# Optimization experiments

Measured on AMD Instinct MI355X. Metric: run time of the kernel, lower is better.

The kernel has to match this reference:

```python
import jax, jax.numpy as jnp
import numpy as np

ALPHA = 32.0
RANK = 256
SCALE = ALPHA / RANK


def setup_inputs() -> dict:
    key = jax.random.key(0)
    k1, k2, k3, k4 = jax.random.split(key, 4)
    x = jax.random.normal(k1, (4, 2048, 4096), dtype=jnp.float32)
    A = jax.random.normal(k2, (256, 4096), dtype=jnp.float32)   # (rank, in)
    B = jax.random.normal(k3, (4096, 256), dtype=jnp.float32)   # (out, rank)
    d_A = jnp.ones((256,), dtype=jnp.float32)                    # init = ones (as in module)
    d_B = jax.random.normal(k4, (4096,), dtype=jnp.float32)      # perturbed for a nontrivial test
    return {"x": x, "A": A, "B": B, "d_A": d_A, "d_B": d_B}


def reference(x, A, B, d_A, d_B):
    # Effective weight: diag(d_B) @ B @ diag(d_A) @ A  -> (out, in)
    scaled_A = d_A[:, None] * A                 # (rank, in)
    BA = B @ scaled_A                            # (out, in)
    W_vera = d_B[:, None] * BA                   # (out, in)
    # out = x @ W_vera.T * scale  -> (..., out)
    return jnp.einsum('bsi,oi->bso', x, W_vera) * SCALE
```

## Files before the change

kernel.cpp:

```cpp
#include <hip/hip_runtime.h>
#include <hip/hip_bf16.h>


#define SCALE_F 0.125f
#define M_TOT 8192
#define K_IN 4096
#define RANK 256
#define N_OUT 4096
#define S_SPLIT 4
#define KC 1024

typedef __bf16 bf16_t;
typedef __bf16 bf16x8 __attribute__((ext_vector_type(8)));
typedef __bf16 bf16x4 __attribute__((ext_vector_type(4)));
typedef float f32x4 __attribute__((ext_vector_type(4)));

typedef __attribute__((address_space(3))) unsigned int lds_u32_t;
typedef const __attribute__((address_space(1))) unsigned int glob_u32_t;

__device__ __forceinline__ void async16(const void* g, void* l) {
    __builtin_amdgcn_global_load_lds((glob_u32_t*)g, (lds_u32_t*)l, 16, 0, 0);
}

__global__ __launch_bounds__(256) void conv_A(const float* __restrict__ A,
                                              const float* __restrict__ dA,
                                              bf16_t* __restrict__ Ab) {
    int idx = blockIdx.x * 256 + threadIdx.x;
    float4 v = ((const float4*)A)[idx];
    float s = dA[idx >> 10];
    bf16x4 o;
    o.x = (bf16_t)(v.x * s); o.y = (bf16_t)(v.y * s);
    o.z = (bf16_t)(v.z * s); o.w = (bf16_t)(v.w * s);
    ((bf16x4*)Ab)[idx] = o;
}

__global__ __launch_bounds__(256) void conv_B(const float* __restrict__ B,
                                              bf16_t* __restrict__ Bb) {
    int idx = blockIdx.x * 256 + threadIdx.x;
    float4 v = ((const float4*)B)[idx];
    bf16x4 o;
    o.x = (bf16_t)v.x; o.y = (bf16_t)v.y; o.z = (bf16_t)v.z; o.w = (bf16_t)v.w;
    ((bf16x4*)Bb)[idx] = o;
}

__global__ __launch_bounds__(256) void gemm1(const float* __restrict__ x,
                                             const bf16_t* __restrict__ Ab,
                                             bf16_t* __restrict__ part) {
    __shared__ bf16_t sX[2][64 * 64];
    __shared__ bf16_t sA[2][128 * 64];
    const int tid = threadIdx.x;
    const int lane = tid & 63, wave = tid >> 6;
    const int wm = wave >> 1, wn = wave & 1;
    const int l15 = lane & 15, quad = lane >> 4;
    const int bm = blockIdx.x * 64;
    const int bn = blockIdx.y * 128;
    const int k0 = blockIdx.z * KC;

    f32x4 acc[2][4];
    const f32x4 zero = {0.f, 0.f, 0.f, 0.f};
    #pragma unroll
    for (int i = 0; i < 2; i++)
        #pragma unroll
        for (int j = 0; j < 4; j++) acc[i][j] = zero;

    f32x4 xr[2][2];

    auto issue_x = [&](int kk) {
        #pragma unroll
        for (int c = 0; c < 2; c++) {
            int idx = c * 256 + tid;
            int row = idx >> 3, sl = idx & 7;
            const float* sp = &x[(size_t)(bm + row) * K_IN + kk + sl * 8];
            xr[c][0] = *(const f32x4*)sp;
            xr[c][1] = *(const f32x4*)(sp + 4);
        }
    };
    auto stage_a = [&](int b, int kk) {
        #pragma unroll
        for (int c = 0; c < 4; c++) {
            int idx = c * 256 + tid;
            int row = idx >> 3, sl = idx & 7;
            async16(&Ab[(size_t)(bn + row) * K_IN + kk + ((sl ^ (row & 7)) << 3)],
                    &sA[b][idx * 8]);
        }
    };
    auto write_x = [&](int b) {
        #pragma unroll
        for (int c = 0; c < 2; c++) {
            int idx = c * 256 + tid;
            int row = idx >> 3, sl = idx & 7;
            bf16x8 o;
            #pragma unroll
            for (int e = 0; e < 4; e++) {
                o[e]     = (bf16_t)xr[c][0][e];
                o[e + 4] = (bf16_t)xr[c][1][e];
            }
            *(bf16x8*)&sX[b][row * 64 + ((sl ^ (row & 7)) << 3)] = o;
        }
    };
    auto compute = [&](int b) {
        #pragma unroll
        for (int ks = 0; ks < 2; ks++) {
            bf16x8 af[2], bfr[4];
            #pragma unroll
            for (int i = 0; i < 2; i++) {
                int row = wm * 32 + i * 16 + l15;
                af[i] = *(const bf16x8*)&sX[b][row * 64 + ((((ks << 2) | quad) ^ (row & 7)) << 3)];
            }
            #pragma unroll
            for (int j = 0; j < 4; j++) {
                int row = wn * 64 + j * 16 + l15;
                bfr[j] = *(const bf16x8*)&sA[b][row * 64 + ((((ks << 2) | quad) ^ (row & 7)) << 3)];
            }
            #pragma unroll
            for (int i = 0; i < 2; i++)
                #pragma unroll
                for (int j = 0; j < 4; j++)
                    acc[i][j] = __builtin_amdgcn_mfma_f32_16x16x32_bf16(af[i], bfr[j], acc[i][j], 0, 0, 0);
        }
    };

    issue_x(k0);
    stage_a(0, k0);
    write_x(0);
    __syncthreads();

    int cur = 0;
    for (int it = 1; it < KC / 64; ++it) {
        const int nxt = cur ^ 1;
        const int kk = k0 + it * 64;
        issue_x(kk);
        stage_a(nxt, kk);
        compute(cur);
        write_x(nxt);
        __syncthreads();
        cur = nxt;
    }
    compute(cur);

    bf16_t* p = part + (size_t)blockIdx.z * (M_TOT * RANK);
    #pragma unroll
    for (int i = 0; i < 2; i++) {
        #pragma unroll
        for (int j = 0; j < 4; j++) {
            int col = bn + wn * 64 + j * 16 + l15;
            #pragma unroll
            for (int r = 0; r < 4; r++) {
                int row = bm + wm * 32 + i * 16 + quad * 4 + r;
                p[(size_t)row * RANK + col] = (bf16_t)acc[i][j][r];
            }
        }
    }
}

__global__ __launch_bounds__(256) void reduce_t(const bf16_t* __restrict__ part,
                                                bf16_t* __restrict__ t) {
    int i = (blockIdx.x * 256 + threadIdx.x) * 8;
    float s[8] = {0.f, 0.f, 0.f, 0.f, 0.f, 0.f, 0.f, 0.f};
    #pragma unroll
    for (int z = 0; z < S_SPLIT; z++) {
        bf16x8 v = *(const bf16x8*)&part[(size_t)z * M_TOT * RANK + i];
        #pragma unroll
        for (int e = 0; e < 8; e++) s[e] += (float)v[e];
    }
    bf16x8 o;
    #pragma unroll
    for (int e = 0; e < 8; e++) o[e] = (bf16_t)s[e];
    *(bf16x8*)&t[i] = o;
}

__global__ __launch_bounds__(256) void gemm2(const bf16_t* __restrict__ t,
                                             const bf16_t* __restrict__ Bb,
                                             const float* __restrict__ dB,
                                             float* __restrict__ out) {
    __shared__ bf16_t sT[2][128 * 64];
    __shared__ bf16_t sB[2][128 * 64];
    const int tid = threadIdx.x;
    const int lane = tid & 63, wave = tid >> 6;
    const int wm = wave >> 1, wn = wave & 1;
    const int l15 = lane & 15, quad = lane >> 4;
    const int bm = blockIdx.x * 128;
    const int bn = blockIdx.y * 128;

    f32x4 acc[4][4];
    const f32x4 zero = {0.f, 0.f, 0.f, 0.f};
    #pragma unroll
    for (int i = 0; i < 4; i++)
        #pragma unroll
        for (int j = 0; j < 4; j++) acc[i][j] = zero;

    auto stage = [&](int b, int kt) {
        #pragma unroll
        for (int c = 0; c < 4; c++) {
            int idx = c * 256 + tid;
            int row = idx >> 3, sl = idx & 7;
            async16(&t[(size_t)(bm + row) * RANK + kt + ((sl ^ (row & 7)) << 3)],
                    &sT[b][idx * 8]);
        }
        #pragma unroll
        for (int c = 0; c < 4; c++) {
            int idx = c * 256 + tid;
            int row = idx >> 3, sl = idx & 7;
            async16(&Bb[(size_t)(bn + row) * RANK + kt + ((sl ^ (row & 7)) << 3)],
                    &sB[b][idx * 8]);
        }
    };
    auto compute = [&](int b) {
        #pragma unroll
        for (int ks = 0; ks < 2; ks++) {
            bf16x8 af[4], bfr[4];
            #pragma unroll
            for (int i = 0; i < 4; i++) {
                int row = wm * 64 + i * 16 + l15;
                af[i] = *(const bf16x8*)&sT[b][row * 64 + ((((ks << 2) | quad) ^ (row & 7)) << 3)];
            }
            #pragma unroll
            for (int j = 0; j < 4; j++) {
                int row = wn * 64 + j * 16 + l15;
                bfr[j] = *(const bf16x8*)&sB[b][row * 64 + ((((ks << 2) | quad) ^ (row & 7)) << 3)];
            }
            #pragma unroll
            for (int i = 0; i < 4; i++)
                #pragma unroll
                for (int j = 0; j < 4; j++)
                    acc[i][j] = __builtin_amdgcn_mfma_f32_16x16x32_bf16(af[i], bfr[j], acc[i][j], 0, 0, 0);
        }
    };

    stage(0, 0);
    __syncthreads();
    int cur = 0;
    #pragma unroll
    for (int it = 1; it < RANK / 64; ++it) {
        stage(cur ^ 1, it * 64);
        compute(cur);
        __syncthreads();
        cur ^= 1;
    }
    compute(cur);

    #pragma unroll
    for (int j = 0; j < 4; j++) {
        int col = bn + wn * 64 + j * 16 + l15;
        float db = dB[col] * SCALE_F;
        #pragma unroll
        for (int i = 0; i < 4; i++) {
            #pragma unroll
            for (int r = 0; r < 4; r++) {
                int row = bm + wm * 64 + i * 16 + quad * 4 + r;
                out[(size_t)row * N_OUT + col] = db * acc[i][j][r];
            }
        }
    }
}

extern "C" void kernel_launch(void* const* d_in, const int* in_sizes, int n_in,
                              void* d_out, int out_size, void* d_ws, size_t ws_size,
                              hipStream_t stream) {
    const float* x  = (const float*)d_in[0];
    const float* A  = (const float*)d_in[1];
    const float* B  = (const float*)d_in[2];
    const float* dA = (const float*)d_in[3];
    const float* dB = (const float*)d_in[4];
    float* out = (float*)d_out;

    char* ws = (char*)d_ws;
    bf16_t* Ab   = (bf16_t*)ws;
    bf16_t* Bb   = (bf16_t*)(ws + (1u << 21));
    bf16_t* tt   = (bf16_t*)(ws + (1u << 22));
    bf16_t* part = (bf16_t*)(ws + (1u << 23));

    conv_A<<<1024, 256, 0, stream>>>(A, dA, Ab);
    conv_B<<<1024, 256, 0, stream>>>(B, Bb);
    gemm1<<<dim3(128, 2, S_SPLIT), 256, 0, stream>>>(x, Ab, part);
    reduce_t<<<1024, 256, 0, stream>>>(part, tt);
    gemm2<<<dim3(64, 32), 256, 0, stream>>>(tt, Bb, dB, out);
}
```

Baseline: 328.6 us.

## Swap MFMA operands for vectorized row stores, halve gemm2 N tile, merge conversions

Both GEMMs now pass the operands to the MFMA in swapped order, so each lane holds four consecutive output columns of one row. This lets the epilogues write bf16x4 and float4 vectors in place of scattered scalar stores, and gemm2 now loads dB as a vector too. gemm2's N tile is halved from 128 to 64, doubling the grid to give more blocks and less LDS and registers per block, at the cost of reloading the T tile twice as often. The two fp32-to-bf16 conversion kernels are merged into one launch.

```diff
diff --git a/kernel.cpp b/kernel.cpp
--- a/kernel.cpp
+++ b/kernel.cpp
@@ -22,25 +22,28 @@
     __builtin_amdgcn_global_load_lds((glob_u32_t*)g, (lds_u32_t*)l, 16, 0, 0);
 }
 
-__global__ __launch_bounds__(256) void conv_A(const float* __restrict__ A,
-                                              const float* __restrict__ dA,
-                                              bf16_t* __restrict__ Ab) {
-    int idx = blockIdx.x * 256 + threadIdx.x;
-    float4 v = ((const float4*)A)[idx];
-    float s = dA[idx >> 10];
-    bf16x4 o;
-    o.x = (bf16_t)(v.x * s); o.y = (bf16_t)(v.y * s);
-    o.z = (bf16_t)(v.z * s); o.w = (bf16_t)(v.w * s);
-    ((bf16x4*)Ab)[idx] = o;
-}
-
-__global__ __launch_bounds__(256) void conv_B(const float* __restrict__ B,
-                                              bf16_t* __restrict__ Bb) {
-    int idx = blockIdx.x * 256 + threadIdx.x;
-    float4 v = ((const float4*)B)[idx];
-    bf16x4 o;
-    o.x = (bf16_t)v.x; o.y = (bf16_t)v.y; o.z = (bf16_t)v.z; o.w = (bf16_t)v.w;
-    ((bf16x4*)Bb)[idx] = o;
+__global__ __launch_bounds__(256) void conv_AB(const float* __restrict__ A,
+                                               const float* __restrict__ dA,
+                                               const float* __restrict__ B,
+                                               bf16_t* __restrict__ Ab,
+                                               bf16_t* __restrict__ Bb) {
+    int b = blockIdx.x;
+    if (b < 1024) {
+        int idx = b * 256 + threadIdx.x;
+        float4 v = ((const float4*)A)[idx];
+        float s = dA[idx >> 10];
+        bf16x4 o;
+        o.x = (bf16_t)(v.x * s); o.y = (bf16_t)(v.y * s);
+        o.z = (bf16_t)(v.z * s); o.w = (bf16_t)(v.w * s);
+        ((bf16x4*)Ab)[idx] = o;
+    } else {
+        int idx = (b - 1024) * 256 + threadIdx.x;
+        float4 v = ((const float4*)B)[idx];
+        bf16x4 o;
+        o.x = (bf16_t)v.x; o.y = (bf16_t)v.y;
+        o.z = (bf16_t)v.z; o.w = (bf16_t)v.w;
+        ((bf16x4*)Bb)[idx] = o;
+    }
 }
 
 __global__ __launch_bounds__(256) void gemm1(const float* __restrict__ x,
@@ -116,7 +119,7 @@
             for (int i = 0; i < 2; i++)
                 #pragma unroll
                 for (int j = 0; j < 4; j++)
-                    acc[i][j] = __builtin_amdgcn_mfma_f32_16x16x32_bf16(af[i], bfr[j], acc[i][j], 0, 0, 0);
+                    acc[i][j] = __builtin_amdgcn_mfma_f32_16x16x32_bf16(bfr[j], af[i], acc[i][j], 0, 0, 0);
         }
     };
 
@@ -141,14 +144,14 @@
     bf16_t* p = part + (size_t)blockIdx.z * (M_TOT * RANK);
     #pragma unroll
     for (int i = 0; i < 2; i++) {
+        int row = bm + wm * 32 + i * 16 + l15;
         #pragma unroll
         for (int j = 0; j < 4; j++) {
-            int col = bn + wn * 64 + j * 16 + l15;
-            #pragma unroll
-            for (int r = 0; r < 4; r++) {
-                int row = bm + wm * 32 + i * 16 + quad * 4 + r;
-                p[(size_t)row * RANK + col] = (bf16_t)acc[i][j][r];
-            }
+            int col = bn + wn * 64 + j * 16 + quad * 4;
+            bf16x4 o;
+            #pragma unroll
+            for (int r = 0; r < 4; r++) o[r] = (bf16_t)acc[i][j][r];
+            *(bf16x4*)&p[(size_t)row * RANK + col] = o;
         }
     }
 }
@@ -174,20 +177,20 @@
                                              const float* __restrict__ dB,
                                              float* __restrict__ out) {
     __shared__ bf16_t sT[2][128 * 64];
-    __shared__ bf16_t sB[2][128 * 64];
+    __shared__ bf16_t sB[2][64 * 64];
     const int tid = threadIdx.x;
     const int lane = tid & 63, wave = tid >> 6;
     const int wm = wave >> 1, wn = wave & 1;
     const int l15 = lane & 15, quad = lane >> 4;
     const int bm = blockIdx.x * 128;
-    const int bn = blockIdx.y * 128;
-
-    f32x4 acc[4][4];
+    const int bn = blockIdx.y * 64;
+
+    f32x4 acc[4][2];
     const f32x4 zero = {0.f, 0.f, 0.f, 0.f};
     #pragma unroll
     for (int i = 0; i < 4; i++)
         #pragma unroll
-        for (int j = 0; j < 4; j++) acc[i][j] = zero;
+        for (int j = 0; j < 2; j++) acc[i][j] = zero;
 
     auto stage = [&](int b, int kt) {
         #pragma unroll
@@ -198,7 +201,7 @@
                     &sT[b][idx * 8]);
         }
         #pragma unroll
-        for (int c = 0; c < 4; c++) {
+        for (int c = 0; c < 2; c++) {
             int idx = c * 256 + tid;
             int row = idx >> 3, sl = idx & 7;
             async16(&Bb[(size_t)(bn + row) * RANK + kt + ((sl ^ (row & 7)) << 3)],
@@ -208,22 +211,22 @@
     auto compute = [&](int b) {
         #pragma unroll
         for (int ks = 0; ks < 2; ks++) {
-            bf16x8 af[4], bfr[4];
+            bf16x8 af[4], bfr[2];
             #pragma unroll
             for (int i = 0; i < 4; i++) {
                 int row = wm * 64 + i * 16 + l15;
                 af[i] = *(const bf16x8*)&sT[b][row * 64 + ((((ks << 2) | quad) ^ (row & 7)) << 3)];
             }
             #pragma unroll
-            for (int j = 0; j < 4; j++) {
-                int row = wn * 64 + j * 16 + l15;
+            for (int j = 0; j < 2; j++) {
+                int row = wn * 32 + j * 16 + l15;
                 bfr[j] = *(const bf16x8*)&sB[b][row * 64 + ((((ks << 2) | quad) ^ (row & 7)) << 3)];
             }
             #pragma unroll
             for (int i = 0; i < 4; i++)
                 #pragma unroll
-                for (int j = 0; j < 4; j++)
-                    acc[i][j] = __builtin_amdgcn_mfma_f32_16x16x32_bf16(af[i], bfr[j], acc[i][j], 0, 0, 0);
+                for (int j = 0; j < 2; j++)
+                    acc[i][j] = __builtin_amdgcn_mfma_f32_16x16x32_bf16(bfr[j], af[i], acc[i][j], 0, 0, 0);
         }
     };
 
@@ -240,16 +243,16 @@
     compute(cur);
 
     #pragma unroll
-    for (int j = 0; j < 4; j++) {
-        int col = bn + wn * 64 + j * 16 + l15;
-        float db = dB[col] * SCALE_F;
-        #pragma unroll
-        for (int i = 0; i < 4; i++) {
-            #pragma unroll
-            for (int r = 0; r < 4; r++) {
-                int row = bm + wm * 64 + i * 16 + quad * 4 + r;
-                out[(size_t)row * N_OUT + col] = db * acc[i][j][r];
-            }
+    for (int i = 0; i < 4; i++) {
+        int row = bm + wm * 64 + i * 16 + l15;
+        #pragma unroll
+        for (int j = 0; j < 2; j++) {
+            int col = bn + wn * 32 + j * 16 + quad * 4;
+            f32x4 db = *(const f32x4*)&dB[col];
+            f32x4 o;
+            #pragma unroll
+            for (int r = 0; r < 4; r++) o[r] = db[r] * SCALE_F * acc[i][j][r];
+            *(f32x4*)&out[(size_t)row * N_OUT + col] = o;
         }
     }
 }
@@ -270,9 +273,8 @@
     bf16_t* tt   = (bf16_t*)(ws + (1u << 22));
     bf16_t* part = (bf16_t*)(ws + (1u << 23));
 
-    conv_A<<<1024, 256, 0, stream>>>(A, dA, Ab);
-    conv_B<<<1024, 256, 0, stream>>>(B, Bb);
+    conv_AB<<<2048, 256, 0, stream>>>(A, dA, B, Ab, Bb);
     gemm1<<<dim3(128, 2, S_SPLIT), 256, 0, stream>>>(x, Ab, part);
     reduce_t<<<1024, 256, 0, stream>>>(part, tt);
-    gemm2<<<dim3(64, 32), 256, 0, stream>>>(tt, Bb, dB, out);
-}
+    gemm2<<<dim3(64, 64), 256, 0, stream>>>(tt, Bb, dB, out);
+}
```

Result: faster. 319.7 us (-2.7%).
